# Kernel tuning notes

Measured on AMD Instinct MI355X. Metric: run time of the kernel, lower is better.

## Reference

```python
import jax, jax.numpy as jnp
import numpy as np

DIM = 768
NUM_HEADS = 16
HEAD_DIM = DIM // NUM_HEADS
SCALE = HEAD_DIM ** -0.5


def setup_inputs() -> dict:
    key = jax.random.key(0)
    ks = jax.random.split(key, 9)
    B, S = 4, 2048
    init = 1.0 / np.sqrt(DIM)
    x = jax.random.normal(ks[0], (B, S, DIM), dtype=jnp.float32)
    Wq = jax.random.uniform(ks[1], (DIM, DIM), jnp.float32, -init, init)
    bq = jax.random.uniform(ks[2], (DIM,), jnp.float32, -init, init)
    Wk = jax.random.uniform(ks[3], (DIM, DIM), jnp.float32, -init, init)
    bk = jax.random.uniform(ks[4], (DIM,), jnp.float32, -init, init)
    Wv = jax.random.uniform(ks[5], (DIM, DIM), jnp.float32, -init, init)
    bv = jax.random.uniform(ks[6], (DIM,), jnp.float32, -init, init)
    Wo = jax.random.uniform(ks[7], (DIM, DIM), jnp.float32, -init, init)
    bo = jax.random.uniform(ks[8], (DIM,), jnp.float32, -init, init)
    return {"x": x, "Wq": Wq, "bq": bq, "Wk": Wk, "bk": bk,
            "Wv": Wv, "bv": bv, "Wo": Wo, "bo": bo}


def reference(x, Wq, bq, Wk, bk, Wv, bv, Wo, bo):
    B, S, D = x.shape
    H, Hd = NUM_HEADS, HEAD_DIM
    # Linear layers (torch Linear: y = x @ W^T + b); split heads -> [B,H,S,Hd]
    q = (x @ Wq.T + bq).reshape(B, S, H, Hd).transpose(0, 2, 1, 3)
    k = (x @ Wk.T + bk).reshape(B, S, H, Hd).transpose(0, 2, 1, 3)
    v = (x @ Wv.T + bv).reshape(B, S, H, Hd).transpose(0, 2, 1, 3)
    scores = jnp.einsum('bhqd,bhkd->bhqk', q, k) * SCALE  # [B,H,S,S]
    attn = jax.nn.softmax(scores, axis=-1)
    # dropout is identity in eval mode
    out = jnp.einsum('bhqk,bhkd->bhqd', attn, v)
    out = out.transpose(0, 2, 1, 3).reshape(B, S, D)
    return out @ Wo.T + bo
```

## Files before the change

### kernel.cpp

```cpp
#include <hip/hip_runtime.h>

typedef __bf16 bf16_t;
typedef bf16_t bf16x8 __attribute__((ext_vector_type(8)));
typedef _Float16 f16_t;
typedef __fp16 hf16x2 __attribute__((ext_vector_type(2)));
typedef f16_t f16x8 __attribute__((ext_vector_type(8)));
typedef float floatx4 __attribute__((ext_vector_type(4)));
typedef float floatx16 __attribute__((ext_vector_type(16)));

#define S_LEN 2048
#define DIM 768
#define NH 16
#define HD 48
#define HDP 64
#define BHEADS 64
#define ATT_SCALE 0.14433756729740643f
#define W_ELEMS (DIM * DIM)

typedef unsigned short u16;
typedef unsigned int u32;

__device__ __forceinline__ u16 f2b(float f) {
  union { float f; u32 i; } z; z.f = f;
  u32 i = z.i;
  return (u16)((i + 0x7fffu + ((i >> 16) & 1u)) >> 16);
}
__device__ __forceinline__ u32 pack2(float a, float b) {
  return (u32)f2b(a) | ((u32)f2b(b) << 16);
}
__device__ __forceinline__ u32 pkrtz2(float a, float b) {
  union { hf16x2 h; u32 u; } z;
  z.h = __builtin_amdgcn_cvt_pkrtz(a, b);
  return z.u;
}
__device__ __forceinline__ void pl32swap(u32& a, u32& b) {
  asm("v_permlane32_swap_b32 %0, %1" : "+v"(a), "+v"(b));
}

__global__ __launch_bounds__(256) void cvt_f32_bf16(
    const float* __restrict__ src, u16* __restrict__ dst)
{
  int idx = blockIdx.x * 256 + threadIdx.x;
  const float4* s = (const float4*)src;
  float4 a = s[idx * 2], b = s[idx * 2 + 1];
  *(uint4*)&dst[(size_t)idx * 8] =
      make_uint4(pack2(a.x, a.y), pack2(a.z, a.w), pack2(b.x, b.y), pack2(b.z, b.w));
}

__global__ __launch_bounds__(256) void cvt_weights(
    const float* __restrict__ w0, const float* __restrict__ w1,
    const float* __restrict__ w2, const float* __restrict__ w3,
    u16* __restrict__ dst)
{
  const float* srcs[4] = {w0, w1, w2, w3};
  const float* src = srcs[blockIdx.y];
  u16* d = dst + (size_t)blockIdx.y * W_ELEMS;
  int idx = blockIdx.x * 256 + threadIdx.x;
  const float4* s = (const float4*)src;
  float4 a = s[idx * 2], b = s[idx * 2 + 1];
  *(uint4*)&d[(size_t)idx * 8] =
      make_uint4(pack2(a.x, a.y), pack2(a.z, a.w), pack2(b.x, b.y), pack2(b.z, b.w));
}

template<int OMODE>
__global__ __launch_bounds__(256) void gemm_bt(
    const u16* __restrict__ A, const u16* __restrict__ W,
    const float* __restrict__ bias, void* __restrict__ outv, float scale)
{
  __shared__ __attribute__((aligned(16))) u16 smem[8704];
  u16 (*As)[40] = (u16(*)[40])smem;
  u16 (*Bs)[40] = (u16(*)[40])(smem + 5120);

  const int tid = threadIdx.x;
  const int w = tid >> 6, lane = tid & 63, lo = lane & 15, quad = lane >> 4;
  const int bm = blockIdx.x & 63, bn = blockIdx.x >> 6;
  const int m0 = bm * 128, n0 = bn * 64;

  floatx4 acc[2][4];
#pragma unroll
  for (int mi = 0; mi < 2; mi++)
#pragma unroll
    for (int ni = 0; ni < 4; ni++) acc[mi][ni] = (floatx4){0.f, 0.f, 0.f, 0.f};

  for (int k0 = 0; k0 < DIM; k0 += 32) {
#pragma unroll
    for (int it = 0; it < 2; ++it) {
      int c = tid + it * 256;
      int r = c >> 2, cc = c & 3;
      const u16* src;
      if constexpr (OMODE == 1) {
        int row = m0 + r, c8 = k0 + cc * 8;
        int h = c8 / HD, d = c8 - h * HD;
        int b = row >> 11, s = row & 2047;
        src = &A[((size_t)((b * NH + h) * S_LEN + s)) * HD + d];
      } else {
        src = &A[(size_t)(m0 + r) * DIM + k0 + cc * 8];
      }
      *(uint4*)&As[r][cc * 8] = *(const uint4*)src;
    }
    {
      int r = tid >> 2, cc = tid & 3;
      *(uint4*)&Bs[r][cc * 8] = *(const uint4*)&W[(size_t)(n0 + r) * DIM + k0 + cc * 8];
    }
    __syncthreads();
    bf16x8 af[2], bfr[4];
#pragma unroll
    for (int mi = 0; mi < 2; mi++) af[mi] = *(const bf16x8*)&As[w * 32 + mi * 16 + lo][quad * 8];
#pragma unroll
    for (int ni = 0; ni < 4; ni++) bfr[ni] = *(const bf16x8*)&Bs[ni * 16 + lo][quad * 8];
#pragma unroll
    for (int mi = 0; mi < 2; mi++)
#pragma unroll
      for (int ni = 0; ni < 4; ni++)
        acc[mi][ni] = __builtin_amdgcn_mfma_f32_16x16x32_bf16(af[mi], bfr[ni], acc[mi][ni], 0, 0, 0);
    __syncthreads();
  }

  if constexpr (OMODE == 2) {
    u16 (*T)[136] = (u16(*)[136])smem;
    u16* out = (u16*)outv;
#pragma unroll
    for (int mi = 0; mi < 2; mi++)
#pragma unroll
      for (int ni = 0; ni < 4; ni++) {
        int col = ni * 16 + lo;
        float bb = bias[n0 + col];
        float v0 = acc[mi][ni][0] + bb, v1 = acc[mi][ni][1] + bb;
        float v2 = acc[mi][ni][2] + bb, v3 = acc[mi][ni][3] + bb;
        *(uint2*)&T[col][w * 32 + mi * 16 + quad * 4] =
            make_uint2(pkrtz2(v0, v1), pkrtz2(v2, v3));
      }
    __syncthreads();
    const int b = m0 >> 11, s0 = m0 & 2047;
#pragma unroll
    for (int it = 0; it < 4; ++it) {
      int ch = tid + it * 256;
      int col = ch >> 4, sc = ch & 15;
      int gcol = n0 + col;
      int h = gcol / HD, d = gcol - h * HD;
      size_t dst = ((size_t)(b * NH + h) * HDP + d) * S_LEN + s0 + sc * 8;
      *(uint4*)&out[dst] = *(const uint4*)&T[col][sc * 8];
    }
    return;
  }

#pragma unroll
  for (int mi = 0; mi < 2; mi++)
#pragma unroll
    for (int ni = 0; ni < 4; ni++)
#pragma unroll
      for (int r = 0; r < 4; r++) {
        int row = m0 + w * 32 + mi * 16 + quad * 4 + r;
        int col = n0 + ni * 16 + lo;
        float v = (acc[mi][ni][r] + bias[col]) * scale;
        if constexpr (OMODE == 1) {
          ((float*)outv)[(size_t)row * DIM + col] = v;
        } else {
          int b = row >> 11, s = row & 2047;
          int h = col / HD, d = col - h * HD;
          ((u16*)outv)[((size_t)((b * NH + h) * S_LEN + s)) * HDP + d] = f2b(v);
        }
      }
}

#define STG_LOAD(k0n) do {                                                     \
  _Pragma("unroll")                                                            \
  for (int it = 0; it < 3; ++it) {                                             \
    int c = tid + it * 256;                                                    \
    if (c < 384) {                                                             \
      int r = c / 6, cc = c - r * 6;                                           \
      stg[it] = *(const uint4*)&K[base + (size_t)((k0n) + r) * HDP + cc * 8];  \
    } else {                                                                   \
      int c2 = c - 384, r = c2 >> 3, cc = c2 & 7;                              \
      stg[it] = *(const uint4*)&V[base + (size_t)r * S_LEN + (k0n) + cc * 8];  \
    }                                                                          \
  }                                                                            \
} while (0)

#define STG_WRITE(bufi) do {                                                   \
  _Pragma("unroll")                                                            \
  for (int it = 0; it < 3; ++it) {                                             \
    int c = tid + it * 256;                                                    \
    if (c < 384) {                                                             \
      int r = c / 6, cc = c - r * 6;                                           \
      *(uint4*)&Ks[bufi][r][cc * 8] = stg[it];                                 \
    } else {                                                                   \
      int c2 = c - 384, r = c2 >> 3, cc = c2 & 7;                              \
      *(uint4*)&Vt[bufi][r][cc * 8] = stg[it];                                 \
    }                                                                          \
  }                                                                            \
} while (0)

__global__ __launch_bounds__(256, 2) void attn_kernel(
    const u16* __restrict__ Q, const u16* __restrict__ K,
    const u16* __restrict__ V, u16* __restrict__ O)
{
  __shared__ __attribute__((aligned(16))) u16 Ks[2][64][56];
  __shared__ __attribute__((aligned(16))) u16 Vt[2][64][72];

  const int tid = threadIdx.x;
  const int w = tid >> 6, lane = tid & 63, l31 = lane & 31, hi = lane >> 5;
  const int flat = blockIdx.x;
  const int xcd = flat & 7, sub = flat >> 3;
  const int bh = xcd * 8 + (sub >> 3);
  const int q0 = (sub & 7) * 256;
  const size_t base = (size_t)bh * S_LEN * HDP;

  bf16x8 qf[2][3];
#pragma unroll
  for (int t = 0; t < 2; t++)
#pragma unroll
    for (int ks = 0; ks < 3; ks++)
      qf[t][ks] = *(const bf16x8*)
          &Q[base + (size_t)(q0 + w * 64 + t * 32 + l31) * HDP + ks * 16 + hi * 8];

  floatx16 oacc[2][2];
#pragma unroll
  for (int t = 0; t < 2; t++)
#pragma unroll
    for (int nd = 0; nd < 2; nd++)
#pragma unroll
      for (int r = 0; r < 16; r++) oacc[t][nd][r] = 0.f;

  float l_lane[2] = {0.f, 0.f};

  uint4 stg[3];
  STG_LOAD(0);
  STG_WRITE(0);

  for (int ti = 0; ti < 32; ++ti) {
    const int cur = ti & 1;
    if (ti < 31) STG_LOAD((ti + 1) * 64);
    __syncthreads();

    bf16x8 ak[2][3];
#pragma unroll
    for (int na = 0; na < 2; na++)
#pragma unroll
      for (int ks = 0; ks < 3; ks++)
        ak[na][ks] = *(const bf16x8*)&Ks[cur][na * 32 + l31][ks * 16 + hi * 8];

    u32 pk[2][2][8];
#pragma unroll
    for (int t = 0; t < 2; t++) {
      floatx16 s0, s1;
#pragma unroll
      for (int r = 0; r < 16; r++) { s0[r] = 0.f; s1[r] = 0.f; }
#pragma unroll
      for (int ks = 0; ks < 3; ks++) {
        s0 = __builtin_amdgcn_mfma_f32_32x32x16_bf16(ak[0][ks], qf[t][ks], s0, 0, 0, 0);
        s1 = __builtin_amdgcn_mfma_f32_32x32x16_bf16(ak[1][ks], qf[t][ks], s1, 0, 0, 0);
      }
#pragma unroll
      for (int m = 0; m < 8; m++) {
        float a0 = __expf(s0[2 * m]), a1 = __expf(s0[2 * m + 1]);
        float b0 = __expf(s1[2 * m]), b1 = __expf(s1[2 * m + 1]);
        l_lane[t] += (a0 + a1) + (b0 + b1);
        pk[t][0][m] = pkrtz2(a0, a1);
        pk[t][1][m] = pkrtz2(b0, b1);
      }
    }

#pragma unroll
    for (int kt = 0; kt < 4; kt++) {
      f16x8 bv0 = *(const f16x8*)&Vt[cur][l31][kt * 16 + hi * 8];
      f16x8 bv1 = *(const f16x8*)&Vt[cur][32 + l31][kt * 16 + hi * 8];
      const int na = kt >> 1, k4 = (kt & 1) * 4;
#pragma unroll
      for (int t = 0; t < 2; t++) {
        u32 w0 = pk[t][na][k4 + 0], w2 = pk[t][na][k4 + 2];
        u32 w1 = pk[t][na][k4 + 1], w3 = pk[t][na][k4 + 3];
        pl32swap(w0, w2);
        pl32swap(w1, w3);
        union { u32 u[4]; f16x8 f; } af;
        af.u[0] = w0; af.u[1] = w1; af.u[2] = w2; af.u[3] = w3;
        oacc[t][0] = __builtin_amdgcn_mfma_f32_32x32x16_f16(af.f, bv0, oacc[t][0], 0, 0, 0);
        oacc[t][1] = __builtin_amdgcn_mfma_f32_32x32x16_f16(af.f, bv1, oacc[t][1], 0, 0, 0);
      }
    }

    if (ti < 31) STG_WRITE(cur ^ 1);
  }

  const size_t obase = (size_t)bh * S_LEN * HD;
  float lt_full[2];
#pragma unroll
  for (int t = 0; t < 2; t++)
    lt_full[t] = l_lane[t] + __shfl_xor(l_lane[t], 32);
#pragma unroll
  for (int t = 0; t < 2; t++) {
#pragma unroll
    for (int r = 0; r < 16; r++) {
      int q_local = (r & 3) + 8 * (r >> 2) + 4 * hi;
      float l_r = __shfl(lt_full[t], q_local);
      float inv = 1.f / l_r;
      int q = q0 + w * 64 + t * 32 + q_local;
      u16* orow = O + obase + (size_t)q * HD;
      orow[l31] = f2b(oacc[t][0][r] * inv);
      if (l31 < 16) orow[32 + l31] = f2b(oacc[t][1][r] * inv);
    }
  }
}

extern "C" void kernel_launch(void* const* d_in, const int* in_sizes, int n_in,
                              void* d_out, int out_size, void* d_ws, size_t ws_size,
                              hipStream_t stream)
{
  const float* x  = (const float*)d_in[0];
  const float* Wq = (const float*)d_in[1];
  const float* bq = (const float*)d_in[2];
  const float* Wk = (const float*)d_in[3];
  const float* bk = (const float*)d_in[4];
  const float* Wv = (const float*)d_in[5];
  const float* bv = (const float*)d_in[6];
  const float* Wo = (const float*)d_in[7];
  const float* bo = (const float*)d_in[8];

  u16* ws   = (u16*)d_ws;
  const size_t qkv_elems = (size_t)BHEADS * S_LEN * HDP;
  u16* q_ws = ws;
  u16* k_ws = q_ws + qkv_elems;
  u16* v_ws = k_ws + qkv_elems;
  u16* x_bf = v_ws + qkv_elems;
  u16* a_ws = x_bf;
  u16* w_bf = x_bf + (size_t)8192 * DIM;

  cvt_f32_bf16<<<dim3(3072), dim3(256), 0, stream>>>(x, x_bf);
  cvt_weights<<<dim3(288, 4), dim3(256), 0, stream>>>(Wq, Wk, Wv, Wo, w_bf);
  u16* wq_bf = w_bf;
  u16* wk_bf = w_bf + (size_t)W_ELEMS;
  u16* wv_bf = w_bf + (size_t)2 * W_ELEMS;
  u16* wo_bf = w_bf + (size_t)3 * W_ELEMS;

  gemm_bt<0><<<dim3(768), dim3(256), 0, stream>>>(x_bf, wq_bf, bq, q_ws, ATT_SCALE);
  gemm_bt<0><<<dim3(768), dim3(256), 0, stream>>>(x_bf, wk_bf, bk, k_ws, 1.0f);
  gemm_bt<2><<<dim3(768), dim3(256), 0, stream>>>(x_bf, wv_bf, bv, v_ws, 1.0f);
  attn_kernel<<<dim3(512), dim3(256), 0, stream>>>(q_ws, k_ws, v_ws, a_ws);
  gemm_bt<1><<<dim3(768), dim3(256), 0, stream>>>(a_ws, wo_bf, bo, d_out, 1.0f);
}
```

Baseline: 276.4 us.

## Fuse QKV projections into one launch with larger double-buffered GEMM tiles

Replaces the three separate Q/K/V projection GEMM launches with a single kernel whose grid covers all three weight matrices. Each block now computes a 128x128 tile instead of 128x64. Shared memory is double-buffered, with register prefetch of the next K-slice overlapping the MFMA work. The output projection gets the same larger tile and pipelined loop. This aims to cut launch count and raise data reuse per block, at the cost of more registers and LDS per block, which may lower occupancy, and fewer blocks for the Wo GEMM.

```diff
diff --git a/kernel.cpp b/kernel.cpp
--- a/kernel.cpp
+++ b/kernel.cpp
@@ -62,104 +62,202 @@
       make_uint4(pack2(a.x, a.y), pack2(a.z, a.w), pack2(b.x, b.y), pack2(b.z, b.w));
 }
 
-template<int OMODE>
-__global__ __launch_bounds__(256) void gemm_bt(
-    const u16* __restrict__ A, const u16* __restrict__ W,
-    const float* __restrict__ bias, void* __restrict__ outv, float scale)
-{
-  __shared__ __attribute__((aligned(16))) u16 smem[8704];
-  u16 (*As)[40] = (u16(*)[40])smem;
-  u16 (*Bs)[40] = (u16(*)[40])(smem + 5120);
+#define AS(buf) ((u16(*)[40])(smem + (buf) * 10240))
+#define BS(buf) ((u16(*)[40])(smem + (buf) * 10240 + 5120))
+
+__global__ __launch_bounds__(256, 2) void gemm_qkv(
+    const u16* __restrict__ A, const u16* __restrict__ Wbase,
+    const float* __restrict__ bq, const float* __restrict__ bk,
+    const float* __restrict__ bv,
+    u16* __restrict__ q_out, u16* __restrict__ k_out, u16* __restrict__ v_out)
+{
+  __shared__ __attribute__((aligned(16))) u16 smem[20480];
 
   const int tid = threadIdx.x;
   const int w = tid >> 6, lane = tid & 63, lo = lane & 15, quad = lane >> 4;
+  const int wr = w >> 1, wc = w & 1;
   const int bm = blockIdx.x & 63, bn = blockIdx.x >> 6;
-  const int m0 = bm * 128, n0 = bn * 64;
-
-  floatx4 acc[2][4];
-#pragma unroll
-  for (int mi = 0; mi < 2; mi++)
+  const int mat = bn / 6;
+  const int n0 = (bn - mat * 6) * 128;
+  const int m0 = bm * 128;
+  const u16* W = Wbase + (size_t)mat * W_ELEMS;
+  const float* bias = mat == 0 ? bq : (mat == 1 ? bk : bv);
+  const float scale = mat == 0 ? ATT_SCALE : 1.0f;
+
+  floatx4 acc[4][4];
+#pragma unroll
+  for (int mi = 0; mi < 4; mi++)
 #pragma unroll
     for (int ni = 0; ni < 4; ni++) acc[mi][ni] = (floatx4){0.f, 0.f, 0.f, 0.f};
 
-  for (int k0 = 0; k0 < DIM; k0 += 32) {
-#pragma unroll
-    for (int it = 0; it < 2; ++it) {
-      int c = tid + it * 256;
-      int r = c >> 2, cc = c & 3;
-      const u16* src;
-      if constexpr (OMODE == 1) {
-        int row = m0 + r, c8 = k0 + cc * 8;
-        int h = c8 / HD, d = c8 - h * HD;
-        int b = row >> 11, s = row & 2047;
-        src = &A[((size_t)((b * NH + h) * S_LEN + s)) * HD + d];
-      } else {
-        src = &A[(size_t)(m0 + r) * DIM + k0 + cc * 8];
-      }
-      *(uint4*)&As[r][cc * 8] = *(const uint4*)src;
-    }
-    {
-      int r = tid >> 2, cc = tid & 3;
-      *(uint4*)&Bs[r][cc * 8] = *(const uint4*)&W[(size_t)(n0 + r) * DIM + k0 + cc * 8];
+  uint4 ga[2], gb[2];
+#pragma unroll
+  for (int it = 0; it < 2; ++it) {
+    int c = tid + it * 256, r = c >> 2, cc = c & 3;
+    ga[it] = *(const uint4*)&A[(size_t)(m0 + r) * DIM + cc * 8];
+    gb[it] = *(const uint4*)&W[(size_t)(n0 + r) * DIM + cc * 8];
+  }
+#pragma unroll
+  for (int it = 0; it < 2; ++it) {
+    int c = tid + it * 256, r = c >> 2, cc = c & 3;
+    *(uint4*)&AS(0)[r][cc * 8] = ga[it];
+    *(uint4*)&BS(0)[r][cc * 8] = gb[it];
+  }
+
+  for (int ks = 0; ks < 24; ++ks) {
+    const int cur = ks & 1;
+    if (ks < 23) {
+      const int kn = (ks + 1) * 32;
+#pragma unroll
+      for (int it = 0; it < 2; ++it) {
+        int c = tid + it * 256, r = c >> 2, cc = c & 3;
+        ga[it] = *(const uint4*)&A[(size_t)(m0 + r) * DIM + kn + cc * 8];
+        gb[it] = *(const uint4*)&W[(size_t)(n0 + r) * DIM + kn + cc * 8];
+      }
     }
     __syncthreads();
-    bf16x8 af[2], bfr[4];
-#pragma unroll
-    for (int mi = 0; mi < 2; mi++) af[mi] = *(const bf16x8*)&As[w * 32 + mi * 16 + lo][quad * 8];
-#pragma unroll
-    for (int ni = 0; ni < 4; ni++) bfr[ni] = *(const bf16x8*)&Bs[ni * 16 + lo][quad * 8];
-#pragma unroll
-    for (int mi = 0; mi < 2; mi++)
+    bf16x8 af[4], bfr[4];
+#pragma unroll
+    for (int mi = 0; mi < 4; mi++) af[mi] = *(const bf16x8*)&AS(cur)[wr * 64 + mi * 16 + lo][quad * 8];
+#pragma unroll
+    for (int ni = 0; ni < 4; ni++) bfr[ni] = *(const bf16x8*)&BS(cur)[wc * 64 + ni * 16 + lo][quad * 8];
+#pragma unroll
+    for (int mi = 0; mi < 4; mi++)
 #pragma unroll
       for (int ni = 0; ni < 4; ni++)
         acc[mi][ni] = __builtin_amdgcn_mfma_f32_16x16x32_bf16(af[mi], bfr[ni], acc[mi][ni], 0, 0, 0);
+    if (ks < 23) {
+      const int nb = cur ^ 1;
+#pragma unroll
+      for (int it = 0; it < 2; ++it) {
+        int c = tid + it * 256, r = c >> 2, cc = c & 3;
+        *(uint4*)&AS(nb)[r][cc * 8] = ga[it];
+        *(uint4*)&BS(nb)[r][cc * 8] = gb[it];
+      }
+    }
+  }
+
+  if (mat < 2) {
+    u16* out = mat == 0 ? q_out : k_out;
+#pragma unroll
+    for (int mi = 0; mi < 4; mi++)
+#pragma unroll
+      for (int ni = 0; ni < 4; ni++)
+#pragma unroll
+        for (int r = 0; r < 4; r++) {
+          int row = m0 + wr * 64 + mi * 16 + quad * 4 + r;
+          int col = n0 + wc * 64 + ni * 16 + lo;
+          float v = (acc[mi][ni][r] + bias[col]) * scale;
+          int b = row >> 11, s = row & 2047;
+          int h = col / HD, d = col - h * HD;
+          out[((size_t)((b * NH + h) * S_LEN + s)) * HDP + d] = f2b(v);
+        }
+  } else {
     __syncthreads();
-  }
-
-  if constexpr (OMODE == 2) {
     u16 (*T)[136] = (u16(*)[136])smem;
-    u16* out = (u16*)outv;
-#pragma unroll
-    for (int mi = 0; mi < 2; mi++)
+#pragma unroll
+    for (int mi = 0; mi < 4; mi++)
 #pragma unroll
       for (int ni = 0; ni < 4; ni++) {
-        int col = ni * 16 + lo;
+        int col = wc * 64 + ni * 16 + lo;
         float bb = bias[n0 + col];
         float v0 = acc[mi][ni][0] + bb, v1 = acc[mi][ni][1] + bb;
         float v2 = acc[mi][ni][2] + bb, v3 = acc[mi][ni][3] + bb;
-        *(uint2*)&T[col][w * 32 + mi * 16 + quad * 4] =
+        *(uint2*)&T[col][wr * 64 + mi * 16 + quad * 4] =
             make_uint2(pkrtz2(v0, v1), pkrtz2(v2, v3));
       }
     __syncthreads();
     const int b = m0 >> 11, s0 = m0 & 2047;
 #pragma unroll
-    for (int it = 0; it < 4; ++it) {
+    for (int it = 0; it < 8; ++it) {
       int ch = tid + it * 256;
       int col = ch >> 4, sc = ch & 15;
       int gcol = n0 + col;
       int h = gcol / HD, d = gcol - h * HD;
       size_t dst = ((size_t)(b * NH + h) * HDP + d) * S_LEN + s0 + sc * 8;
-      *(uint4*)&out[dst] = *(const uint4*)&T[col][sc * 8];
-    }
-    return;
-  }
-
-#pragma unroll
-  for (int mi = 0; mi < 2; mi++)
+      *(uint4*)&v_out[dst] = *(const uint4*)&T[col][sc * 8];
+    }
+  }
+}
+
+__global__ __launch_bounds__(256, 2) void gemm_wo(
+    const u16* __restrict__ A, const u16* __restrict__ W,
+    const float* __restrict__ bias, float* __restrict__ out)
+{
+  __shared__ __attribute__((aligned(16))) u16 smem[20480];
+
+  const int tid = threadIdx.x;
+  const int w = tid >> 6, lane = tid & 63, lo = lane & 15, quad = lane >> 4;
+  const int wr = w >> 1, wc = w & 1;
+  const int bm = blockIdx.x & 63, bn = blockIdx.x >> 6;
+  const int m0 = bm * 128, n0 = bn * 128;
+
+  floatx4 acc[4][4];
+#pragma unroll
+  for (int mi = 0; mi < 4; mi++)
+#pragma unroll
+    for (int ni = 0; ni < 4; ni++) acc[mi][ni] = (floatx4){0.f, 0.f, 0.f, 0.f};
+
+  uint4 ga[2], gb[2];
+#pragma unroll
+  for (int it = 0; it < 2; ++it) {
+    int c = tid + it * 256, r = c >> 2, cc = c & 3;
+    int c8 = cc * 8, h = c8 / HD, d = c8 - h * HD;
+    int row = m0 + r, b = row >> 11, s = row & 2047;
+    ga[it] = *(const uint4*)&A[((size_t)((b * NH + h) * S_LEN + s)) * HD + d];
+    gb[it] = *(const uint4*)&W[(size_t)(n0 + r) * DIM + cc * 8];
+  }
+#pragma unroll
+  for (int it = 0; it < 2; ++it) {
+    int c = tid + it * 256, r = c >> 2, cc = c & 3;
+    *(uint4*)&AS(0)[r][cc * 8] = ga[it];
+    *(uint4*)&BS(0)[r][cc * 8] = gb[it];
+  }
+
+  for (int ks = 0; ks < 24; ++ks) {
+    const int cur = ks & 1;
+    if (ks < 23) {
+      const int kn = (ks + 1) * 32;
+#pragma unroll
+      for (int it = 0; it < 2; ++it) {
+        int c = tid + it * 256, r = c >> 2, cc = c & 3;
+        int c8 = kn + cc * 8, h = c8 / HD, d = c8 - h * HD;
+        int row = m0 + r, b = row >> 11, s = row & 2047;
+        ga[it] = *(const uint4*)&A[((size_t)((b * NH + h) * S_LEN + s)) * HD + d];
+        gb[it] = *(const uint4*)&W[(size_t)(n0 + r) * DIM + kn + cc * 8];
+      }
+    }
+    __syncthreads();
+    bf16x8 af[4], bfr[4];
+#pragma unroll
+    for (int mi = 0; mi < 4; mi++) af[mi] = *(const bf16x8*)&AS(cur)[wr * 64 + mi * 16 + lo][quad * 8];
+#pragma unroll
+    for (int ni = 0; ni < 4; ni++) bfr[ni] = *(const bf16x8*)&BS(cur)[wc * 64 + ni * 16 + lo][quad * 8];
+#pragma unroll
+    for (int mi = 0; mi < 4; mi++)
+#pragma unroll
+      for (int ni = 0; ni < 4; ni++)
+        acc[mi][ni] = __builtin_amdgcn_mfma_f32_16x16x32_bf16(af[mi], bfr[ni], acc[mi][ni], 0, 0, 0);
+    if (ks < 23) {
+      const int nb = cur ^ 1;
+#pragma unroll
+      for (int it = 0; it < 2; ++it) {
+        int c = tid + it * 256, r = c >> 2, cc = c & 3;
+        *(uint4*)&AS(nb)[r][cc * 8] = ga[it];
+        *(uint4*)&BS(nb)[r][cc * 8] = gb[it];
+      }
+    }
+  }
+
+#pragma unroll
+  for (int mi = 0; mi < 4; mi++)
 #pragma unroll
     for (int ni = 0; ni < 4; ni++)
 #pragma unroll
       for (int r = 0; r < 4; r++) {
-        int row = m0 + w * 32 + mi * 16 + quad * 4 + r;
-        int col = n0 + ni * 16 + lo;
-        float v = (acc[mi][ni][r] + bias[col]) * scale;
-        if constexpr (OMODE == 1) {
-          ((float*)outv)[(size_t)row * DIM + col] = v;
-        } else {
-          int b = row >> 11, s = row & 2047;
-          int h = col / HD, d = col - h * HD;
-          ((u16*)outv)[((size_t)((b * NH + h) * S_LEN + s)) * HDP + d] = f2b(v);
-        }
+        int row = m0 + wr * 64 + mi * 16 + quad * 4 + r;
+        int col = n0 + wc * 64 + ni * 16 + lo;
+        out[(size_t)row * DIM + col] = acc[mi][ni][r] + bias[col];
       }
 }
 
@@ -327,14 +425,10 @@
 
   cvt_f32_bf16<<<dim3(3072), dim3(256), 0, stream>>>(x, x_bf);
   cvt_weights<<<dim3(288, 4), dim3(256), 0, stream>>>(Wq, Wk, Wv, Wo, w_bf);
-  u16* wq_bf = w_bf;
-  u16* wk_bf = w_bf + (size_t)W_ELEMS;
-  u16* wv_bf = w_bf + (size_t)2 * W_ELEMS;
   u16* wo_bf = w_bf + (size_t)3 * W_ELEMS;
 
-  gemm_bt<0><<<dim3(768), dim3(256), 0, stream>>>(x_bf, wq_bf, bq, q_ws, ATT_SCALE);
-  gemm_bt<0><<<dim3(768), dim3(256), 0, stream>>>(x_bf, wk_bf, bk, k_ws, 1.0f);
-  gemm_bt<2><<<dim3(768), dim3(256), 0, stream>>>(x_bf, wv_bf, bv, v_ws, 1.0f);
+  gemm_qkv<<<dim3(1152), dim3(256), 0, stream>>>(x_bf, w_bf, bq, bk, bv,
+                                                 q_ws, k_ws, v_ws);
   attn_kernel<<<dim3(512), dim3(256), 0, stream>>>(q_ws, k_ws, v_ws, a_ws);
-  gemm_bt<1><<<dim3(768), dim3(256), 0, stream>>>(a_ws, wo_bf, bo, d_out, 1.0f);
-}
+  gemm_wo<<<dim3(384), dim3(256), 0, stream>>>(a_ws, wo_bf, bo, (float*)d_out);
+}
```

After: 377.0 us. 36.4% more time.
